# Kernel tuning notes

Measured on AMD Instinct MI355X. Metric: run time of the kernel, lower is better.

## Reference

```python
import jax, jax.numpy as jnp
import numpy as np

# Dimensions
NT, NS = 1000, 2048   # timesteps, basins
NF, NG = 6, 32        # forcing channels, static attributes
NH, NR, HS = 16, 8, 256  # buckets, routing taps, hidden size
NK, NGD = 3, 9        # len(kDict)=3 (km,ki,ke), len(gDict)=9


def setup_inputs() -> dict:
    key = jax.random.key(0)
    ks = jax.random.split(key, 16)
    # Physically plausible forcings: Prcp/Evp nonnegative, T1<=T2 (min/max temp)
    Prcp = jax.random.uniform(ks[0], (NT, NS)) * 10.0
    Evp = jax.random.uniform(ks[1], (NT, NS)) * 5.0
    Tm = jax.random.normal(ks[2], (NT, NS)) * 10.0
    T1 = Tm - jax.random.uniform(ks[3], (NT, NS)) * 5.0
    T2 = Tm + jax.random.uniform(ks[4], (NT, NS)) * 5.0
    Rad = jax.random.uniform(ks[5], (NT, NS))
    Hum = jax.random.uniform(ks[6], (NT, NS))
    x = jnp.stack([Prcp, Evp, T1, T2, Rad, Hum], axis=-1)  # [nt, ns, 6]
    xc = jax.random.normal(ks[7], (NS, NG))

    def lin(k, fan_in, fan_out, s=0.05):
        k1, k2 = jax.random.split(k)
        return (jax.random.normal(k1, (fan_in, fan_out)) * s,
                jax.random.normal(k2, (fan_out,)) * s)

    W_fc, b_fc = lin(ks[8], NG, HS)
    W_r, b_r = lin(ks[9], HS, NH * (NR + 1))
    W_g, b_g = lin(ks[10], HS, NH * NGD)
    W_kin, b_kin = lin(ks[11], 4, HS)
    W_kout, b_kout = lin(ks[12], HS, NH * NK)
    return dict(x=x, xc=xc, W_fc=W_fc, b_fc=b_fc, W_r=W_r, b_r=b_r,
                W_g=W_g, b_g=b_g, W_kin=W_kin, b_kin=b_kin,
                W_kout=W_kout, b_kout=b_kout)


def _hardsigmoid(v):
    return jnp.clip(v / 6.0 + 0.5, 0.0, 1.0)


def _forward(x, xc, W_fc, b_fc, W_r, b_r, W_g, b_g, W_kin, b_kin, W_kout, b_kout):
    nt, ns, _ = x.shape
    Prcp, Evp, T1, T2 = x[..., 0], x[..., 1], x[..., 2], x[..., 3]
    f = x[..., 2:]                        # [nt, ns, 4] (T1,T2,Rad,Hum)

    # ---- getParam (eval mode: DropMask is identity) ----
    state = xc @ W_fc + b_fc              # [ns, hs]
    pK = jnp.tanh(f @ W_kin + b_kin + state) @ W_kout + b_kout  # [nt, ns, nh*3]
    hG = jnp.tanh(state)
    pG = hG @ W_g + b_g                   # [ns, nh*9]
    pR = hG @ W_r + b_r                   # [ns, nh*(nr+1)]

    # sepParam(K): km=exp, ki=relu, ke=exp  -> time-varying [nt, ns, nh]
    km = jnp.exp(pK[..., 0 * NH:1 * NH])
    ki = jax.nn.relu(pK[..., 1 * NH:2 * NH])
    ke = jnp.exp(pK[..., 2 * NH:3 * NH])

    # sepParam(G): static [ns, nh]
    g = lambda i: pG[..., i * NH:(i + 1) * NH]
    kp = jax.nn.sigmoid(g(0))
    ks_ = jax.nn.sigmoid(g(1))
    kd = jax.nn.sigmoid(g(2))
    gd = jax.nn.sigmoid(g(3))
    gl = (jax.nn.sigmoid(g(4)) * 10.0) ** 3
    qb = jax.nn.relu(g(5)) / 10.0
    ga = jax.nn.softmax(g(6), axis=-1)    # area weights over buckets
    gi = _hardsigmoid(g(7)) / 2.0
    ge = jax.nn.relu(g(8))

    # onePeakWeight: unimodal routing weights [ns, nh, nr]
    r = pR.reshape(ns, NH, NR + 1)
    s = jax.nn.softmax(r, axis=-1)
    c = jnp.cumsum(s, axis=-1)
    w = jnp.minimum(c, 1.0 - c + s)[..., :NR]
    wr = w / jnp.sum(w, axis=-1, keepdims=True)

    # divideP: snow/liquid split from min/max temperature crossing 0 C
    fl = jnp.clip(T2 / (T2 - T1 + 1e-5), 0.0, 1.0)  # liquid fraction
    Pl = (Prcp * fl)[..., None]           # [nt, ns, 1]
    Ps = (Prcp * (1.0 - fl))[..., None]
    Ev = Evp[..., None]

    # ---- bucket.step recurrence over time (the custom-scan hot loop) ----
    def step(carry, inp):
        Sf, Ss, Sg = carry                # each [ns, nh]
        Ps_t, Pl_t, Ev_t, km_t, ki_t, ke_t = inp
        # snow bucket: accumulate, melt capped by degree-day factor km
        Sf = Sf + Ps_t
        qf = jnp.minimum(Sf, km_t)
        Sf = Sf - qf
        # partition inflow: impervious/direct fraction gi
        inflow = qf + Pl_t
        qd = inflow * gi
        Ss = Ss + inflow * (1.0 - gi)
        # evapotranspiration
        E = jnp.minimum(jnp.maximum(Ss, 0.0), Ev_t * ke_t * ge)
        Ss = Ss - E
        # interflow capped by ki
        qi = jnp.minimum(ki_t, jnp.maximum(Ss, 0.0))
        Ss = Ss - qi
        # quick flow above capacity gl, slow drainage below
        qp = kp * jnp.maximum(Ss - gl, 0.0)
        qsa = ks_ * jnp.clip(Ss, 0.0, gl)
        Ss = Ss - qp - qsa
        # deep/groundwater bucket: fraction gd percolates, linear reservoir kd + baseflow qb
        Sg = Sg + qsa * gd
        qg = kd * Sg + qb
        Sg = Sg * (1.0 - kd)
        q = qp + qsa * (1.0 - gd) + qg + qd + qi
        return (Sf, Ss, Sg), q

    init = (jnp.zeros((ns, NH), x.dtype),
            jnp.zeros((ns, NH), x.dtype),
            jnp.zeros((ns, NH), x.dtype))
    _, Qp = jax.lax.scan(step, init, (Ps, Pl, Ev, km, ki, ke))  # [nt, ns, nh]

    # routing: valid temporal convolution with per-bucket unit hydrograph wr
    Tout = nt - NR + 1
    Q = jnp.zeros((Tout, ns, NH), Qp.dtype)
    for rr in range(NR):  # NR is a small fixed constant
        Q = Q + Qp[NR - 1 - rr: nt - rr] * wr[..., rr]
    yOut = jnp.sum(Q * ga, axis=-1)       # [Tout, ns]
    return yOut


def reference(x, xc, W_fc, b_fc, W_r, b_r, W_g, b_g, W_kin, b_kin, W_kout, b_kout):
    return _forward(x, xc, W_fc, b_fc, W_r, b_r, W_g, b_g, W_kin, b_kin, W_kout, b_kout)
```

## Files before the change

### kernel.cpp

```cpp
#include <hip/hip_runtime.h>
#include <hip/hip_bf16.h>

#define NT   1000
#define NS   2048
#define NH   16
#define NR   8
#define HS   256
#define TOUT 993

typedef __attribute__((ext_vector_type(8))) short short8;
typedef __attribute__((ext_vector_type(4))) float f32x4;

__device__ __forceinline__ ushort f2bf(float f) {
    union { float f; unsigned int u; } v; v.f = f;
    unsigned int u = v.u;
    return (ushort)((u + 0x7fffu + ((u >> 16) & 1u)) >> 16);
}
__device__ __forceinline__ float bf2f(ushort u) {
    union { unsigned int i; float f; } v; v.i = ((unsigned int)u) << 16; return v.f;
}
__device__ __forceinline__ unsigned int packbf2(float lo, float hi) {
    union { __hip_bfloat162 b; unsigned int u; } v;
    v.b = __float22bfloat162_rn(make_float2(lo, hi));
    return v.u;
}
__device__ __forceinline__ float sigf(float x) { return 1.f / (1.f + __expf(-x)); }
__device__ __forceinline__ float fast_tanh(float z) {
    float e = exp2f(z * 2.885390082f);
    return 1.f - 2.f * __builtin_amdgcn_rcpf(e + 1.f);
}
template<int CTRL>
__device__ __forceinline__ float dpp_add(float v) {
    int s = __builtin_amdgcn_update_dpp(0, __builtin_bit_cast(int, v), CTRL, 0xf, 0xf, true);
    return v + __builtin_bit_cast(float, s);
}

__global__ __launch_bounds__(256) void kA(
    const float* __restrict__ xc, const float* __restrict__ W_fc, const float* __restrict__ b_fc,
    const float* __restrict__ W_r, const float* __restrict__ b_r,
    const float* __restrict__ W_g, const float* __restrict__ b_g,
    const float* __restrict__ W_kin, const float* __restrict__ b_kin,
    const float* __restrict__ W_kout,
    float* __restrict__ stateK, float* __restrict__ params,
    ushort* __restrict__ Wt_g, ushort* __restrict__ whlo_g)
{
    __shared__ float xcs[32];
    __shared__ float hG[256];
    __shared__ float pGR[288];
    const int s = blockIdx.x, tid = threadIdx.x;

    if (tid < 32) xcs[tid] = xc[s * 32 + tid];
    __syncthreads();

    float acc = b_fc[tid];
#pragma unroll 8
    for (int k = 0; k < 32; ++k) acc = fmaf(xcs[k], W_fc[k * 256 + tid], acc);
    stateK[s * 256 + tid] = acc + b_kin[tid];
    hG[tid] = tanhf(acc);
    __syncthreads();

    for (int j = tid; j < 288; j += 256) {
        const float* W = (j < 144) ? W_g : W_r;
        const float* b = (j < 144) ? b_g : b_r;
        int col = (j < 144) ? j : (j - 144);
        float a = b[col];
#pragma unroll 4
        for (int k = 0; k < 256; ++k) a = fmaf(hG[k], W[k * 144 + col], a);
        pGR[j] = a;
    }
    __syncthreads();

    if (tid < 16) {
        const int h = tid;
        float g0 = pGR[h],       g1 = pGR[16 + h],  g2 = pGR[32 + h];
        float g3 = pGR[48 + h],  g4 = pGR[64 + h],  g5 = pGR[80 + h];
        float g6 = pGR[96 + h],  g7 = pGR[112 + h], g8 = pGR[128 + h];
        float kp = sigf(g0), ksg = sigf(g1), kd = sigf(g2), gd = sigf(g3);
        float t4 = sigf(g4) * 10.f; float gl = t4 * t4 * t4;
        float qb = fmaxf(g5, 0.f) * 0.1f;
        float gi = fminf(fmaxf(g7 * (1.f / 6.f) + 0.5f, 0.f), 1.f) * 0.5f;
        float ge = fmaxf(g8, 0.f);
        float m = g6;
        for (int o = 1; o < 16; o <<= 1) m = fmaxf(m, __shfl_xor(m, o));
        float e = __expf(g6 - m), esum = e;
        for (int o = 1; o < 16; o <<= 1) esum += __shfl_xor(esum, o);
        float ga = e / esum;
        float r[9], rm = -1e30f;
#pragma unroll
        for (int i = 0; i < 9; ++i) { r[i] = pGR[144 + h * 9 + i]; rm = fmaxf(rm, r[i]); }
        float er[9], es = 0.f;
#pragma unroll
        for (int i = 0; i < 9; ++i) { er[i] = __expf(r[i] - rm); es += er[i]; }
        float inv_es = 1.f / es, c = 0.f, wsum = 0.f, w[8];
#pragma unroll
        for (int i = 0; i < 8; ++i) {
            float si = er[i] * inv_es; c += si;
            float wi = fminf(c, 1.f - c + si);
            w[i] = wi; wsum += wi;
        }
        const int base = s * 16 + h;
        params[0 * 32768 + base] = kp;       params[1 * 32768 + base] = ksg;
        params[2 * 32768 + base] = kd;       params[3 * 32768 + base] = gd;
        params[4 * 32768 + base] = gl;       params[5 * 32768 + base] = qb;
        params[6 * 32768 + base] = gi;       params[7 * 32768 + base] = 1.f - gi;
        params[8 * 32768 + base] = 1.f - kd; params[9 * 32768 + base] = 1.f - gd;
        params[10 * 32768 + base] = ge;
        float sc = ga / wsum;
#pragma unroll
        for (int i = 0; i < 8; ++i) params[(11 + i) * 32768 + base] = w[i] * sc;
    }

    if (s == 0) {
        for (int i = tid; i < 48 * 256; i += 256) {
            int col = i % 48, slot = i / 48;
            int kk = slot >> 5, q = (slot >> 3) & 3, j = slot & 7;
            int h = kk * 32 + ((j < 4) ? (q * 4 + j) : (16 + q * 4 + (j - 4)));
            Wt_g[col * 264 + slot] = f2bf(W_kout[h * 48 + col]);
        }
        {
            const int h = tid;
#pragma unroll
            for (int f = 0; f < 4; ++f) {
                float w = W_kin[f * 256 + h];
                ushort hi = f2bf(w);
                float lo = w - bf2f(hi);
                whlo_g[h * 8 + f] = hi;
                whlo_g[h * 8 + 4 + f] = f2bf(lo);
            }
        }
    }
}

__global__ __launch_bounds__(256, 3) void kB(
    const float* __restrict__ x,
    const float* __restrict__ stateK, const float* __restrict__ b_kout,
    const ushort* __restrict__ Wt_g, const ushort* __restrict__ whlo_g,
    const float* __restrict__ params,
    unsigned int* __restrict__ kmki, ushort* __restrict__ kevA,
    float2* __restrict__ pspl)
{
    __shared__ ushort Wt[48 * 264];
    __shared__ float  stS[16 * 260];
    __shared__ ushort whloS[2048];
    __shared__ float  geS[256];
    __shared__ float  evS[4][5][16];
    const int tid = threadIdx.x;
    const int st = blockIdx.x & 127;
    const int tg = blockIdx.x >> 7;
    const int s0 = st << 4;

    for (int i = tid; i < 3168; i += 256)
        ((uint2*)Wt)[i] = ((const uint2*)Wt_g)[i];
#pragma unroll
    for (int i = tid; i < 1024; i += 256) {
        int row = i >> 6, c = (i & 63) << 2;
        *(float4*)(stS + row * 260 + c) = *(const float4*)(stateK + (s0 + row) * 256 + c);
    }
    *(float4*)(whloS + tid * 8) = ((const float4*)whlo_g)[tid];
    geS[tid] = params[10 * 32768 + s0 * 16 + tid];
    __syncthreads();

    const int wv = tid >> 6, lane = tid & 63;
    const int mi = lane & 15, quad = lane >> 4;
    const int site = s0 + mi;
    const int t0 = tg * 20 + wv * 5;

    float xf[5][4];
#pragma unroll
    for (int ti = 0; ti < 5; ++ti) {
        const int t = t0 + ti;
        const int xb = (t * 2048 + site) * 6;
        float2 u23 = *(const float2*)(x + xb + 2);
        float2 u45 = *(const float2*)(x + xb + 4);
        xf[ti][0] = u23.x; xf[ti][1] = u23.y; xf[ti][2] = u45.x; xf[ti][3] = u45.y;
        if (lane < 16) {
            float2 u01 = *(const float2*)(x + xb);
            float fl = fminf(fmaxf(u23.y * __builtin_amdgcn_rcpf(u23.y - u23.x + 1e-5f), 0.f), 1.f);
            const int sg = st * 4 + (mi >> 2), sl = mi & 3;
            pspl[(sg * 1000 + t) * 4 + sl] = make_float2(u01.x * (1.f - fl), u01.x * fl);
            evS[wv][ti][mi] = u01.y;
        }
    }

    unsigned int bfr[5][4];
#pragma unroll
    for (int ti = 0; ti < 5; ++ti) {
        const float x0 = xf[ti][0], x1 = xf[ti][1], x2 = xf[ti][2], x3 = xf[ti][3];
        unsigned int h01 = packbf2(x0, x1), h23 = packbf2(x2, x3);
        float l0 = x0 - bf2f((ushort)(h01 & 0xffffu));
        float l1 = x1 - bf2f((ushort)(h01 >> 16));
        float l2 = x2 - bf2f((ushort)(h23 & 0xffffu));
        float l3 = x3 - bf2f((ushort)(h23 >> 16));
        unsigned int l01 = packbf2(l0, l1), l23 = packbf2(l2, l3);
        bfr[ti][0] = (quad == 0) ? h01 : (quad == 1 ? l01 : 0u);
        bfr[ti][1] = (quad == 0) ? h23 : (quad == 1 ? l23 : 0u);
        bfr[ti][2] = (quad == 0) ? h01 : 0u;
        bfr[ti][3] = (quad == 0) ? h23 : 0u;
    }

    const float*  stp = stS + mi * 260;
    const ushort* Wt0 = Wt + mi * 264 + quad * 8;
    const int q4 = quad * 4;

    f32x4 acc[5][3];
#pragma unroll
    for (int ti = 0; ti < 5; ++ti)
#pragma unroll
        for (int j = 0; j < 3; ++j) acc[ti][j] = (f32x4){0.f, 0.f, 0.f, 0.f};

#pragma unroll 1
    for (int kk = 0; kk < 8; ++kk) {
        const int ko = kk * 32;
        union { short8 s; unsigned int u[4]; } W0, W1, A0, A1;
        W0.s = *(const short8*)(whloS + (ko + mi) * 8);
        W1.s = *(const short8*)(whloS + (ko + 16 + mi) * 8);
        A0.u[0] = (quad <= 1) ? W0.u[0] : 0u;
        A0.u[1] = (quad <= 1) ? W0.u[1] : 0u;
        A0.u[2] = (quad == 0) ? W0.u[2] : 0u;
        A0.u[3] = (quad == 0) ? W0.u[3] : 0u;
        A1.u[0] = (quad <= 1) ? W1.u[0] : 0u;
        A1.u[1] = (quad <= 1) ? W1.u[1] : 0u;
        A1.u[2] = (quad == 0) ? W1.u[2] : 0u;
        A1.u[3] = (quad == 0) ? W1.u[3] : 0u;
        f32x4 c0 = *(const f32x4*)(stp + ko + q4);
        f32x4 c1 = *(const f32x4*)(stp + ko + 16 + q4);
        short8 b0 = *(const short8*)(Wt0 + ko);
        short8 b1 = *(const short8*)(Wt0 + 16 * 264 + ko);
        short8 b2 = *(const short8*)(Wt0 + 32 * 264 + ko);
#pragma unroll
        for (int ti = 0; ti < 5; ++ti) {
            union { short8 s; unsigned int u[4]; } B;
            B.u[0] = bfr[ti][0]; B.u[1] = bfr[ti][1];
            B.u[2] = bfr[ti][2]; B.u[3] = bfr[ti][3];
            f32x4 z0 = __builtin_amdgcn_mfma_f32_16x16x32_bf16(A0.s, B.s, c0, 0, 0, 0);
            f32x4 z1 = __builtin_amdgcn_mfma_f32_16x16x32_bf16(A1.s, B.s, c1, 0, 0, 0);
            float t0_ = fast_tanh(z0[0]), t1_ = fast_tanh(z0[1]);
            float t2_ = fast_tanh(z0[2]), t3_ = fast_tanh(z0[3]);
            float t4_ = fast_tanh(z1[0]), t5_ = fast_tanh(z1[1]);
            float t6_ = fast_tanh(z1[2]), t7_ = fast_tanh(z1[3]);
            union { short8 s; unsigned int u[4]; } a;
            a.u[0] = packbf2(t0_, t1_);
            a.u[1] = packbf2(t2_, t3_);
            a.u[2] = packbf2(t4_, t5_);
            a.u[3] = packbf2(t6_, t7_);
            acc[ti][0] = __builtin_amdgcn_mfma_f32_16x16x32_bf16(a.s, b0, acc[ti][0], 0, 0, 0);
            acc[ti][1] = __builtin_amdgcn_mfma_f32_16x16x32_bf16(a.s, b1, acc[ti][1], 0, 0, 0);
            acc[ti][2] = __builtin_amdgcn_mfma_f32_16x16x32_bf16(a.s, b2, acc[ti][2], 0, 0, 0);
        }
    }

    const float bo0 = b_kout[mi], bo1 = b_kout[16 + mi], bo2 = b_kout[32 + mi];
    const int sgW = st * 4 + quad;
#pragma unroll
    for (int ti = 0; ti < 5; ++ti) {
        const int t = t0 + ti;
#pragma unroll
        for (int reg = 0; reg < 4; ++reg) {
            const int sl = quad * 4 + reg;
            float km = __expf(acc[ti][0][reg] + bo0);
            float ki = fmaxf(acc[ti][1][reg] + bo1, 0.f);
            float ke = __expf(acc[ti][2][reg] + bo2);
            float kev = ke * evS[wv][ti][sl] * geS[sl * 16 + mi];
            const int idx = (sgW * 1000 + t) * 64 + (reg << 4) + mi;
            kmki[idx] = (unsigned int)f2bf(km) | ((unsigned int)f2bf(ki) << 16);
            kevA[idx] = f2bf(kev);
        }
    }
}

__global__ __launch_bounds__(64, 1) void kC(
    const unsigned int* __restrict__ kmki, const ushort* __restrict__ kevA,
    const float2* __restrict__ pspl,
    const float* __restrict__ params, float* __restrict__ yOut)
{
    const int tid = threadIdx.x;
    const int sg = blockIdx.x;
    const int sl = tid >> 4;
    const int s = sg * 4 + sl;
    const int h = tid & 15;
    const int gid = s * 16 + h;

    const float kp  = params[0 * 32768 + gid];
    const float ks_ = params[1 * 32768 + gid];
    const float kd  = params[2 * 32768 + gid];
    const float gd  = params[3 * 32768 + gid];
    const float gl  = params[4 * 32768 + gid];
    const float qbv = params[5 * 32768 + gid];
    const float gi  = params[6 * 32768 + gid];
    const float gi1 = params[7 * 32768 + gid];
    const float kd1 = params[8 * 32768 + gid];
    const float gd1 = params[9 * 32768 + gid];
    float wrga[8];
#pragma unroll
    for (int i = 0; i < 8; ++i) wrga[i] = params[(11 + i) * 32768 + gid];

    float Sf = 0.f, Ss = 0.f, Sg = 0.f;
    float qh[8];
#pragma unroll
    for (int i = 0; i < 8; ++i) qh[i] = 0.f;

    const int base = sg * 1000;

    unsigned int a0[8], a1[8], a2[8]; ushort e0[8], e1[8], e2[8];
    float2 p0[8], p1[8], p2[8];

#define LOADB(B, tb) do {                                               \
        const int _b = base + (tb) * 8;                                 \
        _Pragma("unroll")                                               \
        for (int i = 0; i < 8; ++i) {                                   \
            a##B[i] = kmki[(_b + i) * 64 + tid];                        \
            e##B[i] = kevA[(_b + i) * 64 + tid];                        \
            p##B[i] = pspl[(_b + i) * 4 + sl];                          \
        }                                                               \
    } while (0)

#define COMPUTEB(B, tb) do {                                            \
        float z[8];                                                     \
        _Pragma("unroll")                                               \
        for (int i = 0; i < 8; ++i) {                                   \
            float km = __builtin_bit_cast(float, a##B[i] << 16);        \
            float ki = __builtin_bit_cast(float, a##B[i] & 0xffff0000u);\
            float kev = __builtin_bit_cast(float, ((unsigned int)e##B[i]) << 16); \
            float ps = p##B[i].x, pl = p##B[i].y;                       \
            Sf += ps;                                                   \
            float qf = fminf(Sf, km); Sf -= qf;                         \
            float inflow = qf + pl;                                     \
            float qd = inflow * gi;                                     \
            Ss = fmaf(inflow, gi1, Ss);                                 \
            float E = fminf(Ss, kev); Ss -= E;                          \
            float qi = fminf(ki, Ss); Ss -= qi;                         \
            float qp = kp * fmaxf(Ss - gl, 0.f);                        \
            float qsa = ks_ * fminf(Ss, gl);                            \
            Ss -= qp + qsa;                                             \
            Sg = fmaf(qsa, gd, Sg);                                     \
            float qg = fmaf(kd, Sg, qbv);                               \
            Sg *= kd1;                                                  \
            float q = fmaf(qsa, gd1, qp) + qg + qd + qi;                \
            qh[i] = q;                                                  \
            float v = 0.f;                                              \
            _Pragma("unroll")                                           \
            for (int k = 0; k < 8; ++k) v = fmaf(wrga[k], qh[(i - k) & 7], v); \
            z[i] = v;                                                   \
        }                                                               \
        _Pragma("unroll")                                               \
        for (int i = 0; i < 8; ++i) z[i] = dpp_add<0xB1>(z[i]);         \
        _Pragma("unroll")                                               \
        for (int i = 0; i < 8; ++i) z[i] = dpp_add<0x4E>(z[i]);         \
        _Pragma("unroll")                                               \
        for (int i = 0; i < 8; ++i) z[i] = dpp_add<0x141>(z[i]);        \
        _Pragma("unroll")                                               \
        for (int i = 0; i < 8; ++i) z[i] = dpp_add<0x140>(z[i]);        \
        if (h == 0) {                                                   \
            const int tbase = (tb) * 8;                                 \
            _Pragma("unroll")                                           \
            for (int i = 0; i < 8; ++i) {                               \
                const int t = tbase + i;                                \
                if (t >= 7) yOut[(t - 7) * 2048 + s] = z[i];            \
            }                                                           \
        }                                                               \
    } while (0)

    LOADB(0, 0);
    LOADB(1, 1);
    LOADB(2, 2);

    for (int it = 0; it < 42; ++it) {
        const int tb = it * 3;
        COMPUTEB(0, tb);
        LOADB(0, (tb + 3 <= 124) ? tb + 3 : 124);
        if (tb + 1 < 125) {
            COMPUTEB(1, tb + 1);
            LOADB(1, (tb + 4 <= 124) ? tb + 4 : 124);
        }
        if (tb + 2 < 125) {
            COMPUTEB(2, tb + 2);
            LOADB(2, (tb + 5 <= 124) ? tb + 5 : 124);
        }
    }
#undef LOADB
#undef COMPUTEB
}

extern "C" void kernel_launch(void* const* d_in, const int* in_sizes, int n_in,
                              void* d_out, int out_size, void* d_ws, size_t ws_size,
                              hipStream_t stream) {
    const float* x      = (const float*)d_in[0];
    const float* xc     = (const float*)d_in[1];
    const float* W_fc   = (const float*)d_in[2];
    const float* b_fc   = (const float*)d_in[3];
    const float* W_r    = (const float*)d_in[4];
    const float* b_r    = (const float*)d_in[5];
    const float* W_g    = (const float*)d_in[6];
    const float* b_g    = (const float*)d_in[7];
    const float* W_kin  = (const float*)d_in[8];
    const float* b_kin  = (const float*)d_in[9];
    const float* W_kout = (const float*)d_in[10];
    const float* b_kout = (const float*)d_in[11];
    float* yOut = (float*)d_out;

    char* ws = (char*)d_ws;
    float*  stateK = (float*)(ws + 0);
    float*  params = (float*)(ws + (2 << 20));
    ushort* Wt_g   = (ushort*)(ws + (6 << 20));
    ushort* whlo_g = (ushort*)(ws + (6 << 20) + (64 << 10));
    char*   p      = ws + (6 << 20) + (128 << 10);
    float2* pspl   = (float2*)p;
    unsigned int* kmki = (unsigned int*)(p + 16384000);
    ushort* kevA   = (ushort*)(p + 16384000 + 131072000);

    hipLaunchKernelGGL(kA, dim3(2048), dim3(256), 0, stream,
                       xc, W_fc, b_fc, W_r, b_r, W_g, b_g, W_kin, b_kin, W_kout,
                       stateK, params, Wt_g, whlo_g);
    hipLaunchKernelGGL(kB, dim3(128 * 50), dim3(256), 0, stream,
                       x, stateK, b_kout, Wt_g, whlo_g, params, kmki, kevA, pspl);
    hipLaunchKernelGGL(kC, dim3(512), dim3(64), 0, stream,
                       kmki, kevA, pspl, params, yOut);
}
```

Baseline: 533.0 us.

## Run recurrence kernel with one basin per block and per-basin intermediate layout

The scan kernel kC now launches one block per basin (2048 blocks) with only 16 active lanes, one per bucket, instead of packing four basins into each 64-lane block. kB writes the km/ki and kev intermediates in a per-basin contiguous layout to match, and the pspl indexing is adjusted. The aim is to put more independent wavefronts on each CU so the latency-bound sequential time loop is better hidden. The cost is that three quarters of each wavefront's lanes sit idle and loads are narrower per wave.

```diff
diff --git a/kernel.cpp b/kernel.cpp
--- a/kernel.cpp
+++ b/kernel.cpp
@@ -234,15 +234,11 @@
             B.u[2] = bfr[ti][2]; B.u[3] = bfr[ti][3];
             f32x4 z0 = __builtin_amdgcn_mfma_f32_16x16x32_bf16(A0.s, B.s, c0, 0, 0, 0);
             f32x4 z1 = __builtin_amdgcn_mfma_f32_16x16x32_bf16(A1.s, B.s, c1, 0, 0, 0);
-            float t0_ = fast_tanh(z0[0]), t1_ = fast_tanh(z0[1]);
-            float t2_ = fast_tanh(z0[2]), t3_ = fast_tanh(z0[3]);
-            float t4_ = fast_tanh(z1[0]), t5_ = fast_tanh(z1[1]);
-            float t6_ = fast_tanh(z1[2]), t7_ = fast_tanh(z1[3]);
             union { short8 s; unsigned int u[4]; } a;
-            a.u[0] = packbf2(t0_, t1_);
-            a.u[1] = packbf2(t2_, t3_);
-            a.u[2] = packbf2(t4_, t5_);
-            a.u[3] = packbf2(t6_, t7_);
+            a.u[0] = packbf2(fast_tanh(z0[0]), fast_tanh(z0[1]));
+            a.u[1] = packbf2(fast_tanh(z0[2]), fast_tanh(z0[3]));
+            a.u[2] = packbf2(fast_tanh(z1[0]), fast_tanh(z1[1]));
+            a.u[3] = packbf2(fast_tanh(z1[2]), fast_tanh(z1[3]));
             acc[ti][0] = __builtin_amdgcn_mfma_f32_16x16x32_bf16(a.s, b0, acc[ti][0], 0, 0, 0);
             acc[ti][1] = __builtin_amdgcn_mfma_f32_16x16x32_bf16(a.s, b1, acc[ti][1], 0, 0, 0);
             acc[ti][2] = __builtin_amdgcn_mfma_f32_16x16x32_bf16(a.s, b2, acc[ti][2], 0, 0, 0);
@@ -250,7 +246,6 @@
     }
 
     const float bo0 = b_kout[mi], bo1 = b_kout[16 + mi], bo2 = b_kout[32 + mi];
-    const int sgW = st * 4 + quad;
 #pragma unroll
     for (int ti = 0; ti < 5; ++ti) {
         const int t = t0 + ti;
@@ -261,7 +256,7 @@
             float ki = fmaxf(acc[ti][1][reg] + bo1, 0.f);
             float ke = __expf(acc[ti][2][reg] + bo2);
             float kev = ke * evS[wv][ti][sl] * geS[sl * 16 + mi];
-            const int idx = (sgW * 1000 + t) * 64 + (reg << 4) + mi;
+            const int idx = ((s0 + sl) * 1000 + t) * 16 + mi;
             kmki[idx] = (unsigned int)f2bf(km) | ((unsigned int)f2bf(ki) << 16);
             kevA[idx] = f2bf(kev);
         }
@@ -274,10 +269,9 @@
     const float* __restrict__ params, float* __restrict__ yOut)
 {
     const int tid = threadIdx.x;
-    const int sg = blockIdx.x;
-    const int sl = tid >> 4;
-    const int s = sg * 4 + sl;
-    const int h = tid & 15;
+    if (tid >= 16) return;
+    const int s = blockIdx.x;
+    const int h = tid;
     const int gid = s * 16 + h;
 
     const float kp  = params[0 * 32768 + gid];
@@ -299,18 +293,20 @@
 #pragma unroll
     for (int i = 0; i < 8; ++i) qh[i] = 0.f;
 
-    const int base = sg * 1000;
+    const int base = s * 1000;
+    const int psb  = (s >> 2) * 4000 + (s & 3);
 
     unsigned int a0[8], a1[8], a2[8]; ushort e0[8], e1[8], e2[8];
     float2 p0[8], p1[8], p2[8];
 
 #define LOADB(B, tb) do {                                               \
         const int _b = base + (tb) * 8;                                 \
+        const int _p = psb + (tb) * 32;                                 \
         _Pragma("unroll")                                               \
         for (int i = 0; i < 8; ++i) {                                   \
-            a##B[i] = kmki[(_b + i) * 64 + tid];                        \
-            e##B[i] = kevA[(_b + i) * 64 + tid];                        \
-            p##B[i] = pspl[(_b + i) * 4 + sl];                          \
+            a##B[i] = kmki[(_b + i) * 16 + h];                          \
+            e##B[i] = kevA[(_b + i) * 16 + h];                          \
+            p##B[i] = pspl[_p + i * 4];                                 \
         }                                                               \
     } while (0)
 
@@ -413,6 +409,6 @@
                        stateK, params, Wt_g, whlo_g);
     hipLaunchKernelGGL(kB, dim3(128 * 50), dim3(256), 0, stream,
                        x, stateK, b_kout, Wt_g, whlo_g, params, kmki, kevA, pspl);
-    hipLaunchKernelGGL(kC, dim3(512), dim3(64), 0, stream,
+    hipLaunchKernelGGL(kC, dim3(2048), dim3(64), 0, stream,
                        kmki, kevA, pspl, params, yOut);
 }
```

Result: slower. 636.1 us (+19.4%).
